# Kernel optimization log

Hardware: AMD Instinct MI355X
Metric: run time of the kernel (lower is better)

## Reference

```python
import jax, jax.numpy as jnp
import numpy as np

DEPTH, DIM, HEADS = 12, 768, 12
B, N = 2, 2048
HEAD_DIM = DIM // HEADS


def setup_inputs() -> dict:
    key = jax.random.key(0)
    ks = jax.random.split(key, 8)
    s = 0.02
    return {
        "x": jax.random.normal(ks[0], (B, N, DIM), jnp.float32),
        "sequence_ids": jnp.sort(jax.random.randint(ks[1], (B, N), 0, 8), axis=-1),
        "sequence_mask": jnp.zeros((B, N), dtype=bool),
        "ln1_w": jnp.ones((DEPTH, DIM), jnp.float32),
        "ln1_b": jnp.zeros((DEPTH, DIM), jnp.float32),
        "qkv_w": jax.random.normal(ks[2], (DEPTH, DIM, 3 * DIM), jnp.float32) * s,
        "qkv_b": jnp.zeros((DEPTH, 3 * DIM), jnp.float32),
        "proj_w": jax.random.normal(ks[3], (DEPTH, DIM, DIM), jnp.float32) * s,
        "proj_b": jnp.zeros((DEPTH, DIM), jnp.float32),
        "ls1_g": jnp.full((DEPTH, DIM), 1e-5, jnp.float32),
        "ln2_w": jnp.ones((DEPTH, DIM), jnp.float32),
        "ln2_b": jnp.zeros((DEPTH, DIM), jnp.float32),
        "fc1_w": jax.random.normal(ks[4], (DEPTH, DIM, 4 * DIM), jnp.float32) * s,
        "fc1_b": jnp.zeros((DEPTH, 4 * DIM), jnp.float32),
        "fc2_w": jax.random.normal(ks[5], (DEPTH, 4 * DIM, DIM), jnp.float32) * s,
        "fc2_b": jnp.zeros((DEPTH, DIM), jnp.float32),
        "ls2_g": jnp.full((DEPTH, DIM), 1e-5, jnp.float32),
        "r": 0,
    }


def _layernorm(x, w, b, eps=1e-5):
    m = x.mean(-1, keepdims=True)
    v = ((x - m) ** 2).mean(-1, keepdims=True)
    return (x - m) * jax.lax.rsqrt(v + eps) * w + b


def _attention(x, attn_mask, qkv_w, qkv_b, proj_w, proj_b):
    b, n, c = x.shape
    qkv = (x @ qkv_w + qkv_b).reshape(b, n, 3, HEADS, HEAD_DIM)
    qkv = jnp.transpose(qkv, (2, 0, 3, 1, 4))  # [3, B, H, N, hd]
    q, k, v = qkv[0], qkv[1], qkv[2]
    attn = jnp.einsum("bhqd,bhkd->bhqk", q, k) * (HEAD_DIM ** -0.5)
    neg_inf = jnp.finfo(attn.dtype).min
    attn = jnp.where(attn_mask[:, None, :, :], neg_inf, attn)  # broadcast over heads
    attn = jax.nn.softmax(attn, axis=-1)
    out = jnp.einsum("bhqk,bhkd->bhqd", attn, v)
    out = jnp.transpose(out, (0, 2, 1, 3)).reshape(b, n, c)
    return out @ proj_w + proj_b


def reference(x, sequence_ids, sequence_mask, ln1_w, ln1_b, qkv_w, qkv_b,
              proj_w, proj_b, ls1_g, ln2_w, ln2_b, fc1_w, fc1_b,
              fc2_w, fc2_b, ls2_g, r):
    # attn_mask: True where attention is NOT allowed
    attn_mask = sequence_ids[:, :, None] != sequence_ids[:, None, :]
    attn_mask = attn_mask | sequence_mask[:, :, None] | sequence_mask[:, None, :]
    for i in range(DEPTH):
        h = _layernorm(x, ln1_w[i], ln1_b[i])
        h = _attention(h, attn_mask, qkv_w[i], qkv_b[i], proj_w[i], proj_b[i])
        x = x + h * ls1_g[i]
        h = _layernorm(x, ln2_w[i], ln2_b[i])
        h = jax.nn.gelu(h @ fc1_w[i] + fc1_b[i], approximate=False) @ fc2_w[i] + fc2_b[i]
        x = x + h * ls2_g[i]
    return x
```

## Files before the change

kernel.cpp:

```cpp
#include <hip/hip_runtime.h>

#define NDEPTH 12
#define NDIM 768
#define NHEADS 12
#define NB 2
#define NSEQ 2048
#define MTOK (NB*NSEQ)

typedef short bf16x8 __attribute__((ext_vector_type(8)));
typedef float f32x4 __attribute__((ext_vector_type(4)));
typedef unsigned short u16;
typedef unsigned int u32;

#define L2E 1.44269504088896f

__device__ inline u16 f2bf(float f){
  union { float f; u32 u; } x; x.f = f;
  u32 r = x.u + 0x7fffu + ((x.u >> 16) & 1u);
  return (u16)(r >> 16);
}

__device__ inline f32x4 mfma16(bf16x8 a, bf16x8 b, f32x4 c){
  return __builtin_amdgcn_mfma_f32_16x16x32_bf16(a, b, c, 0, 0, 0);
}

#define GLOAD_LDS(gsrc, ldst) __builtin_amdgcn_global_load_lds( \
    (const __attribute__((address_space(1))) u32*)(gsrc), \
    (__attribute__((address_space(3))) u32*)(ldst), 16, 0, 0)

__device__ inline void ln_body(const float* __restrict__ x,
    const float* __restrict__ w, const float* __restrict__ b,
    u16* __restrict__ out, int blk){
  int wv = threadIdx.x >> 6, lane = threadIdx.x & 63;
  int row = blk * 4 + wv;
  const float* xr = x + (size_t)row * NDIM;
  float v[12];
  #pragma unroll
  for (int j = 0; j < 3; j++){
    float4 f = *(const float4*)&xr[4*lane + 256*j];
    v[j*4+0] = f.x; v[j*4+1] = f.y; v[j*4+2] = f.z; v[j*4+3] = f.w;
  }
  float s = 0.f;
  #pragma unroll
  for (int j = 0; j < 12; j++) s += v[j];
  #pragma unroll
  for (int m = 1; m < 64; m <<= 1) s += __shfl_xor(s, m);
  float mean = s * (1.0f/768.0f);
  float q = 0.f;
  #pragma unroll
  for (int j = 0; j < 12; j++){ float d = v[j]-mean; q += d*d; }
  #pragma unroll
  for (int m = 1; m < 64; m <<= 1) q += __shfl_xor(q, m);
  float rs = rsqrtf(q * (1.0f/768.0f) + 1e-5f);
  u16* orow = out + (size_t)row * NDIM;
  #pragma unroll
  for (int j = 0; j < 3; j++){
    int c0 = 4*lane + 256*j;
    u16 tmp[4];
    #pragma unroll
    for (int i = 0; i < 4; i++)
      tmp[i] = f2bf((v[j*4+i]-mean)*rs*w[c0+i] + b[c0+i]);
    *(uint2*)&orow[c0] = *(uint2*)tmp;
  }
}

__global__ __launch_bounds__(256) void ln_kernel(const float* __restrict__ x,
    const float* __restrict__ w, const float* __restrict__ b,
    u16* __restrict__ out){
  ln_body(x, w, b, out, blockIdx.x);
}

__device__ inline void wtrans_body(const float* __restrict__ in,
    u16* __restrict__ out, int K, int N, int n0, int k0, float* tile){
  int t = threadIdx.x;
  #pragma unroll
  for (int j = 0; j < 4; j++){
    int idx = t + j*256;
    int r = idx >> 4, c4 = (idx & 15) << 2;
    float4 f = *(const float4*)&in[(size_t)(k0+r)*N + n0 + c4];
    float* tp = &tile[r*65 + c4];
    tp[0] = f.x; tp[1] = f.y; tp[2] = f.z; tp[3] = f.w;
  }
  __syncthreads();
  #pragma unroll
  for (int j = 0; j < 2; j++){
    int idx = t + j*256;
    int c = idx >> 3, r8 = (idx & 7) << 3;
    u16 tmp[8];
    #pragma unroll
    for (int i = 0; i < 8; i++) tmp[i] = f2bf(tile[(r8+i)*65 + c]);
    *(uint4*)&out[(size_t)(n0+c)*K + k0 + r8] = *(uint4*)tmp;
  }
}

__global__ __launch_bounds__(256) void lnwt_kernel(
    const float* __restrict__ x, const float* __restrict__ lw,
    const float* __restrict__ lb, u16* __restrict__ lout,
    const float* __restrict__ qkvw, const float* __restrict__ projw,
    const float* __restrict__ fc1w, const float* __restrict__ fc2w,
    u16* __restrict__ wq, u16* __restrict__ wp,
    u16* __restrict__ w1, u16* __restrict__ w2){
  __shared__ float tile[64*65];
  int bid = blockIdx.x;
  if (bid < 1024){ ln_body(x, lw, lb, lout, bid); return; }
  bid -= 1024;
  const float* in; u16* out; int K, N, tl;
  if (bid < 432){        in = qkvw; out = wq; K = 768;  N = 2304; tl = bid; }
  else if (bid < 576){   in = projw; out = wp; K = 768; N = 768;  tl = bid - 432; }
  else if (bid < 1152){  in = fc1w; out = w1; K = 768;  N = 3072; tl = bid - 576; }
  else {                 in = fc2w; out = w2; K = 3072; N = 768;  tl = bid - 1152; }
  int ntn = N >> 6;
  int n0 = (tl % ntn) << 6, k0 = (tl / ntn) << 6;
  wtrans_body(in, out, K, N, n0, k0, tile);
}

__global__ __launch_bounds__(256) void wtrans_kernel(const float* __restrict__ in,
    u16* __restrict__ out, int K, int N){
  __shared__ float tile[64*65];
  wtrans_body(in, out, K, N, blockIdx.x*64, blockIdx.y*64, tile);
}

template<int BN, int EPI>
__global__ __launch_bounds__(512) void gemm_kernel(
    const u16* __restrict__ A, const u16* __restrict__ Wt,
    const float* __restrict__ bias, const float* __restrict__ g,
    u16* __restrict__ outb, float* __restrict__ xres,
    int M, int N, int K)
{
  constexpr int WGN = BN / 32;
  constexpr int WGM = 8 / WGN;
  constexpr int WTM = 128 / WGM;
  constexpr int MI = WTM / 16;
  constexpr int NI = 2;
  __shared__ u16 As[2][128*64];
  __shared__ u16 Bs[2][BN*64];
  int nwg = gridDim.x;
  int bid = (blockIdx.x & 7) * (nwg >> 3) + (blockIdx.x >> 3);
  int nt = N / BN;
  int bm = bid / nt, bn = bid % nt;
  int m0 = bm*128, n0 = bn*BN;
  int t = threadIdx.x, lane = t & 63, wv = t >> 6;
  int wm = (wv / WGN) * WTM, wn = (wv % WGN) * 32;
  f32x4 acc[MI][NI] = {};
  int fr = lane & 15, fg = lane >> 4;

  auto stage = [&](int bf, int k0){
    #pragma unroll
    for (int i = 0; i < 2; i++){
      int off = t*16 + i*8192;
      int row = off >> 7, cb = off & 127;
      const char* src = (const char*)A + ((size_t)(m0+row)*K + k0)*2 + (cb ^ ((row&7)<<4));
      GLOAD_LDS(src, (char*)As[bf] + off);
    }
    #pragma unroll
    for (int i = 0; i < BN/64; i++){
      int off = t*16 + i*8192;
      int row = off >> 7, cb = off & 127;
      const char* src = (const char*)Wt + ((size_t)(n0+row)*K + k0)*2 + (cb ^ ((row&7)<<4));
      GLOAD_LDS(src, (char*)Bs[bf] + off);
    }
  };

  stage(0, 0);
  int cur = 0;
  for (int k0 = 0; k0 < K; k0 += 64){
    __syncthreads();
    if (k0 + 64 < K) stage(cur ^ 1, k0 + 64);

    bf16x8 af[MI][2], bfv[NI][2];
    #pragma unroll
    for (int mi = 0; mi < MI; mi++)
      #pragma unroll
      for (int kh = 0; kh < 2; kh++){
        int row = wm + mi*16 + fr;
        int off = (row*128 + kh*64 + fg*16) ^ ((row&7)<<4);
        af[mi][kh] = *(const bf16x8*)((const char*)As[cur] + off);
      }
    #pragma unroll
    for (int ni = 0; ni < NI; ni++)
      #pragma unroll
      for (int kh = 0; kh < 2; kh++){
        int row = wn + ni*16 + fr;
        int off = (row*128 + kh*64 + fg*16) ^ ((row&7)<<4);
        bfv[ni][kh] = *(const bf16x8*)((const char*)Bs[cur] + off);
      }
    #pragma unroll
    for (int mi = 0; mi < MI; mi++)
      #pragma unroll
      for (int ni = 0; ni < NI; ni++){
        acc[mi][ni] = mfma16(af[mi][0], bfv[ni][0], acc[mi][ni]);
        acc[mi][ni] = mfma16(af[mi][1], bfv[ni][1], acc[mi][ni]);
      }
    cur ^= 1;
  }

  int fq = fg << 2;
  #pragma unroll
  for (int mi = 0; mi < MI; mi++){
    #pragma unroll
    for (int ni = 0; ni < NI; ni++){
      int col = n0 + wn + ni*16 + fr;
      float bv = bias[col];
      #pragma unroll
      for (int r = 0; r < 4; r++){
        int row = m0 + wm + mi*16 + fq + r;
        float v = acc[mi][ni][r] + bv;
        if (EPI == 0){
          outb[(size_t)row * N + col] = f2bf(v);
        } else if (EPI == 1){
          float ge = 0.5f * v * (1.0f + erff(v * 0.70710678118f));
          outb[(size_t)row * N + col] = f2bf(ge);
        } else {
          xres[(size_t)row * N + col] += v * g[col];
        }
      }
    }
  }
}

__global__ __launch_bounds__(256) void attn_kernel(
    const u16* __restrict__ qkv, const int* __restrict__ sid,
    const unsigned char* __restrict__ smask, u16* __restrict__ outb)
{
  __shared__ u16 Ks[64][72];
  __shared__ u16 Vs[64][72];
  __shared__ u16 Ps[4][16][72];
  int nwg = gridDim.x;
  int blk = (blockIdx.x & 7) * (nwg >> 3) + (blockIdx.x >> 3);
  int qt = blk & 31; int bh = blk >> 5;
  int b = bh / NHEADS, h = bh % NHEADS;
  int t = threadIdx.x, lane = t & 63, wv = t >> 6;
  int q0 = qt << 6;
  size_t rowbase = (size_t)b * NSEQ;
  int fr = lane & 15, fg8 = (lane >> 4) << 3, fq = (lane >> 4) << 2;

  int qrow = q0 + (wv << 4) + fr;
  const u16* qp = qkv + (rowbase + qrow) * 2304 + h*64 + fg8;
  bf16x8 qf0 = *(const bf16x8*)qp;
  bf16x8 qf1 = *(const bf16x8*)(qp + 32);

  int qlo = sid[rowbase + q0];
  int qhi = sid[rowbase + q0 + 63];

  int sq[4]; int mq[4];
  #pragma unroll
  for (int r = 0; r < 4; r++){
    int qr = q0 + (wv << 4) + fq + r;
    sq[r] = sid[rowbase + qr];
    mq[r] = smask[rowbase + qr];
  }
  float m[4], l[4]; f32x4 o[4] = {};
  #pragma unroll
  for (int r = 0; r < 4; r++){ m[r] = -3.0e38f; l[r] = 0.f; }

  int skk = t >> 2, sd = (t & 3) << 4;

  for (int kt = 0; kt < NSEQ/64; kt++){
    int klo = sid[rowbase + (kt << 6)];
    int khi = sid[rowbase + (kt << 6) + 63];
    if (khi < qlo || klo > qhi) continue;

    __syncthreads();
    int krow = (kt << 6) + skk;
    const u16* kp = qkv + (rowbase + krow) * 2304 + 768 + h*64 + sd;
    *(uint4*)&Ks[skk][sd]     = *(const uint4*)kp;
    *(uint4*)&Ks[skk][sd + 8] = *(const uint4*)(kp + 8);
    const u16* vp = kp + 768;
    uint4 v0 = *(const uint4*)vp, v1 = *(const uint4*)(vp + 8);
    {
      const u16* vv = (const u16*)&v0;
      #pragma unroll
      for (int i = 0; i < 8; i++) Vs[sd + i][skk] = vv[i];
      vv = (const u16*)&v1;
      #pragma unroll
      for (int i = 0; i < 8; i++) Vs[sd + 8 + i][skk] = vv[i];
    }
    int ks[4]; int mk[4];
    #pragma unroll
    for (int s2 = 0; s2 < 4; s2++){
      int kk = (kt << 6) + (s2 << 4) + fr;
      ks[s2] = sid[rowbase + kk];
      mk[s2] = smask[rowbase + kk];
    }
    __syncthreads();

    f32x4 S[4];
    #pragma unroll
    for (int s2 = 0; s2 < 4; s2++){
      bf16x8 kf0 = *(const bf16x8*)&Ks[(s2 << 4) + fr][fg8];
      bf16x8 kf1 = *(const bf16x8*)&Ks[(s2 << 4) + fr][fg8 + 32];
      f32x4 s = {};
      s = mfma16(qf0, kf0, s);
      s = mfma16(qf1, kf1, s);
      #pragma unroll
      for (int r = 0; r < 4; r++){
        float v = s[r] * 0.125f;
        bool msk = (mq[r] | mk[s2]) || (sq[r] != ks[s2]);
        S[s2][r] = msk ? -3.0e38f : v;
      }
    }
    float mn[4], sf[4], rs[4];
    #pragma unroll
    for (int r = 0; r < 4; r++){
      float mx = fmaxf(fmaxf(S[0][r], S[1][r]), fmaxf(S[2][r], S[3][r]));
      #pragma unroll
      for (int d = 1; d < 16; d <<= 1) mx = fmaxf(mx, __shfl_xor(mx, d));
      mn[r] = fmaxf(m[r], mx);
      sf[r] = exp2f((m[r] - mn[r]) * L2E);
      rs[r] = 0.f;
    }
    #pragma unroll
    for (int s2 = 0; s2 < 4; s2++){
      #pragma unroll
      for (int r = 0; r < 4; r++){
        float p = exp2f((S[s2][r] - mn[r]) * L2E);
        rs[r] += p;
        Ps[wv][fq + r][(s2 << 4) + fr] = f2bf(p);
      }
    }
    #pragma unroll
    for (int r = 0; r < 4; r++){
      #pragma unroll
      for (int d = 1; d < 16; d <<= 1) rs[r] += __shfl_xor(rs[r], d);
      l[r] = l[r] * sf[r] + rs[r];
      m[r] = mn[r];
    }
    #pragma unroll
    for (int dsub = 0; dsub < 4; dsub++)
      #pragma unroll
      for (int r = 0; r < 4; r++) o[dsub][r] *= sf[r];
    __syncthreads();
    #pragma unroll
    for (int kg = 0; kg < 2; kg++){
      bf16x8 pf = *(const bf16x8*)&Ps[wv][fr][(kg << 5) + fg8];
      #pragma unroll
      for (int dsub = 0; dsub < 4; dsub++){
        bf16x8 vf = *(const bf16x8*)&Vs[(dsub << 4) + fr][(kg << 5) + fg8];
        o[dsub] = mfma16(pf, vf, o[dsub]);
      }
    }
  }

  #pragma unroll
  for (int dsub = 0; dsub < 4; dsub++){
    #pragma unroll
    for (int r = 0; r < 4; r++){
      int row = q0 + (wv << 4) + fq + r;
      int col = h*64 + (dsub << 4) + fr;
      outb[(rowbase + row) * NDIM + col] = f2bf(o[dsub][r] / l[r]);
    }
  }
}

extern "C" void kernel_launch(void* const* d_in, const int* in_sizes, int n_in,
                              void* d_out, int out_size, void* d_ws, size_t ws_size,
                              hipStream_t stream) {
  const float* x_in = (const float*)d_in[0];
  const int* sid = (const int*)d_in[1];
  const unsigned char* smask = (const unsigned char*)d_in[2];
  const float* ln1w = (const float*)d_in[3];
  const float* ln1b = (const float*)d_in[4];
  const float* qkvw = (const float*)d_in[5];
  const float* qkvb = (const float*)d_in[6];
  const float* projw = (const float*)d_in[7];
  const float* projb = (const float*)d_in[8];
  const float* ls1 = (const float*)d_in[9];
  const float* ln2w = (const float*)d_in[10];
  const float* ln2b = (const float*)d_in[11];
  const float* fc1w = (const float*)d_in[12];
  const float* fc1b = (const float*)d_in[13];
  const float* fc2w = (const float*)d_in[14];
  const float* fc2b = (const float*)d_in[15];
  const float* ls2 = (const float*)d_in[16];

  float* x = (float*)d_out;
  char* ws = (char*)d_ws;
  u16* hbuf   = (u16*)ws;
  u16* qkvbuf = (u16*)(ws + (size_t)6291456);
  u16* abuf   = (u16*)(ws + (size_t)25165824);
  u16* mbuf   = (u16*)(ws + (size_t)31457280);
  const size_t WT0 = 56623104;

  bool fused_wt = ws_size >= WT0 + (size_t)14155776;
  u16* wall = (u16*)(ws + WT0);
  u16 *wq, *wp, *w1, *w2;
  if (fused_wt){
    wq = wall; wp = wq + (size_t)2304*768;
    w1 = wp + (size_t)768*768; w2 = w1 + (size_t)768*3072;
  } else {
    wq = wp = w1 = w2 = wall;
  }

  hipMemcpyAsync(x, x_in, (size_t)MTOK*NDIM*4, hipMemcpyDeviceToDevice, stream);

  for (int i = 0; i < NDEPTH; i++){
    const float* qw = qkvw + (size_t)i*NDIM*2304;
    const float* pw = projw + (size_t)i*NDIM*NDIM;
    const float* f1 = fc1w + (size_t)i*NDIM*3072;
    const float* f2 = fc2w + (size_t)i*3072*NDIM;

    if (fused_wt){
      lnwt_kernel<<<2752, 256, 0, stream>>>(x, ln1w + i*NDIM, ln1b + i*NDIM, hbuf,
                                            qw, pw, f1, f2, wq, wp, w1, w2);
    } else {
      ln_kernel<<<MTOK/4, 256, 0, stream>>>(x, ln1w + i*NDIM, ln1b + i*NDIM, hbuf);
      wtrans_kernel<<<dim3(2304/64, 768/64), 256, 0, stream>>>(qw, wq, NDIM, 2304);
    }
    gemm_kernel<128,0><<<(MTOK/128)*(2304/128), 512, 0, stream>>>(
        hbuf, wq, qkvb + (size_t)i*2304, nullptr, qkvbuf, nullptr, MTOK, 2304, NDIM);
    attn_kernel<<<NB*NHEADS*(NSEQ/64), 256, 0, stream>>>(qkvbuf, sid, smask, abuf);
    if (!fused_wt)
      wtrans_kernel<<<dim3(768/64, 768/64), 256, 0, stream>>>(pw, wp, NDIM, NDIM);
    gemm_kernel<64,2><<<(MTOK/128)*(NDIM/64), 512, 0, stream>>>(
        abuf, wp, projb + (size_t)i*NDIM, ls1 + (size_t)i*NDIM,
        nullptr, x, MTOK, NDIM, NDIM);
    ln_kernel<<<MTOK/4, 256, 0, stream>>>(x, ln2w + i*NDIM, ln2b + i*NDIM, hbuf);
    if (!fused_wt)
      wtrans_kernel<<<dim3(3072/64, 768/64), 256, 0, stream>>>(f1, w1, NDIM, 3072);
    gemm_kernel<128,1><<<(MTOK/128)*(3072/128), 512, 0, stream>>>(
        hbuf, w1, fc1b + (size_t)i*3072, nullptr, mbuf, nullptr, MTOK, 3072, NDIM);
    if (!fused_wt)
      wtrans_kernel<<<dim3(768/64, 3072/64), 256, 0, stream>>>(f2, w2, 3072, NDIM);
    gemm_kernel<64,2><<<(MTOK/128)*(NDIM/64), 512, 0, stream>>>(
        mbuf, w2, fc2b + (size_t)i*NDIM, ls2 + (size_t)i*NDIM,
        nullptr, x, MTOK, NDIM, 3072);
  }
}
```

Baseline: 2.080 ms.

## Switch dense GEMMs to FP8 operands with FP8 activations and weights

Converts layernorm outputs, attention outputs, GELU outputs and transposed weights to FP8 (e4m3 via v_cvt_pk_fp8_f32) and runs all four linear layers on the 16x16x32 FP8 MFMA. The LDS tiles and global loads are relaid for 1-byte elements with a smaller swizzle. This halves the bytes moved per GEMM and is meant to double MFMA throughput. It trades precision: the whole residual stream is fed through FP8 quantisation without scaling, which may exceed tolerance.

Measured after the change: 2.292 ms. +10.2%, slower.

```diff
diff --git a/kernel.cpp b/kernel.cpp
--- a/kernel.cpp
+++ b/kernel.cpp
@@ -11,6 +11,8 @@
 typedef float f32x4 __attribute__((ext_vector_type(4)));
 typedef unsigned short u16;
 typedef unsigned int u32;
+typedef unsigned char u8;
+typedef long long i64;
 
 #define L2E 1.44269504088896f
 
@@ -20,6 +22,12 @@
   return (u16)(r >> 16);
 }
 
+__device__ inline u32 cvt2fp8(float lo, float hi){
+  u32 r;
+  asm volatile("v_cvt_pk_fp8_f32 %0, %1, %2" : "=v"(r) : "v"(lo), "v"(hi));
+  return r & 0xffffu;
+}
+
 __device__ inline f32x4 mfma16(bf16x8 a, bf16x8 b, f32x4 c){
   return __builtin_amdgcn_mfma_f32_16x16x32_bf16(a, b, c, 0, 0, 0);
 }
@@ -30,7 +38,7 @@
 
 __device__ inline void ln_body(const float* __restrict__ x,
     const float* __restrict__ w, const float* __restrict__ b,
-    u16* __restrict__ out, int blk){
+    u8* __restrict__ out, int blk){
   int wv = threadIdx.x >> 6, lane = threadIdx.x & 63;
   int row = blk * 4 + wv;
   const float* xr = x + (size_t)row * NDIM;
@@ -52,26 +60,27 @@
   #pragma unroll
   for (int m = 1; m < 64; m <<= 1) q += __shfl_xor(q, m);
   float rs = rsqrtf(q * (1.0f/768.0f) + 1e-5f);
-  u16* orow = out + (size_t)row * NDIM;
+  u8* orow = out + (size_t)row * NDIM;
   #pragma unroll
   for (int j = 0; j < 3; j++){
     int c0 = 4*lane + 256*j;
-    u16 tmp[4];
-    #pragma unroll
-    for (int i = 0; i < 4; i++)
-      tmp[i] = f2bf((v[j*4+i]-mean)*rs*w[c0+i] + b[c0+i]);
-    *(uint2*)&orow[c0] = *(uint2*)tmp;
+    float y0 = (v[j*4+0]-mean)*rs*w[c0+0] + b[c0+0];
+    float y1 = (v[j*4+1]-mean)*rs*w[c0+1] + b[c0+1];
+    float y2 = (v[j*4+2]-mean)*rs*w[c0+2] + b[c0+2];
+    float y3 = (v[j*4+3]-mean)*rs*w[c0+3] + b[c0+3];
+    u32 lo = cvt2fp8(y0, y1), hi = cvt2fp8(y2, y3);
+    *(u32*)&orow[c0] = lo | (hi << 16);
   }
 }
 
 __global__ __launch_bounds__(256) void ln_kernel(const float* __restrict__ x,
     const float* __restrict__ w, const float* __restrict__ b,
-    u16* __restrict__ out){
+    u8* __restrict__ out){
   ln_body(x, w, b, out, blockIdx.x);
 }
 
 __device__ inline void wtrans_body(const float* __restrict__ in,
-    u16* __restrict__ out, int K, int N, int n0, int k0, float* tile){
+    u8* __restrict__ out, int K, int N, int n0, int k0, float* tile){
   int t = threadIdx.x;
   #pragma unroll
   for (int j = 0; j < 4; j++){
@@ -82,29 +91,30 @@
     tp[0] = f.x; tp[1] = f.y; tp[2] = f.z; tp[3] = f.w;
   }
   __syncthreads();
-  #pragma unroll
-  for (int j = 0; j < 2; j++){
-    int idx = t + j*256;
-    int c = idx >> 3, r8 = (idx & 7) << 3;
-    u16 tmp[8];
-    #pragma unroll
-    for (int i = 0; i < 8; i++) tmp[i] = f2bf(tile[(r8+i)*65 + c]);
-    *(uint4*)&out[(size_t)(n0+c)*K + k0 + r8] = *(uint4*)tmp;
-  }
+  int c = t >> 2, r16 = (t & 3) << 4;
+  u32 wds[4];
+  #pragma unroll
+  for (int p = 0; p < 4; p++){
+    u32 lo = cvt2fp8(tile[(r16+4*p+0)*65 + c], tile[(r16+4*p+1)*65 + c]);
+    u32 hi = cvt2fp8(tile[(r16+4*p+2)*65 + c], tile[(r16+4*p+3)*65 + c]);
+    wds[p] = lo | (hi << 16);
+  }
+  uint4 o; o.x = wds[0]; o.y = wds[1]; o.z = wds[2]; o.w = wds[3];
+  *(uint4*)&out[(size_t)(n0+c)*K + k0 + r16] = o;
 }
 
 __global__ __launch_bounds__(256) void lnwt_kernel(
     const float* __restrict__ x, const float* __restrict__ lw,
-    const float* __restrict__ lb, u16* __restrict__ lout,
+    const float* __restrict__ lb, u8* __restrict__ lout,
     const float* __restrict__ qkvw, const float* __restrict__ projw,
     const float* __restrict__ fc1w, const float* __restrict__ fc2w,
-    u16* __restrict__ wq, u16* __restrict__ wp,
-    u16* __restrict__ w1, u16* __restrict__ w2){
+    u8* __restrict__ wq, u8* __restrict__ wp,
+    u8* __restrict__ w1, u8* __restrict__ w2){
   __shared__ float tile[64*65];
   int bid = blockIdx.x;
   if (bid < 1024){ ln_body(x, lw, lb, lout, bid); return; }
   bid -= 1024;
-  const float* in; u16* out; int K, N, tl;
+  const float* in; u8* out; int K, N, tl;
   if (bid < 432){        in = qkvw; out = wq; K = 768;  N = 2304; tl = bid; }
   else if (bid < 576){   in = projw; out = wp; K = 768; N = 768;  tl = bid - 432; }
   else if (bid < 1152){  in = fc1w; out = w1; K = 768;  N = 3072; tl = bid - 576; }
@@ -115,16 +125,16 @@
 }
 
 __global__ __launch_bounds__(256) void wtrans_kernel(const float* __restrict__ in,
-    u16* __restrict__ out, int K, int N){
+    u8* __restrict__ out, int K, int N){
   __shared__ float tile[64*65];
   wtrans_body(in, out, K, N, blockIdx.x*64, blockIdx.y*64, tile);
 }
 
 template<int BN, int EPI>
-__global__ __launch_bounds__(512) void gemm_kernel(
-    const u16* __restrict__ A, const u16* __restrict__ Wt,
+__global__ __launch_bounds__(512) void gemm8_kernel(
+    const u8* __restrict__ A, const u8* __restrict__ Wt,
     const float* __restrict__ bias, const float* __restrict__ g,
-    u16* __restrict__ outb, float* __restrict__ xres,
+    u16* __restrict__ outb, u8* __restrict__ out8, float* __restrict__ xres,
     int M, int N, int K)
 {
   constexpr int WGN = BN / 32;
@@ -132,8 +142,8 @@
   constexpr int WTM = 128 / WGM;
   constexpr int MI = WTM / 16;
   constexpr int NI = 2;
-  __shared__ u16 As[2][128*64];
-  __shared__ u16 Bs[2][BN*64];
+  __shared__ u8 As[2][128*64];
+  __shared__ u8 Bs[2][BN*64];
   int nwg = gridDim.x;
   int bid = (blockIdx.x & 7) * (nwg >> 3) + (blockIdx.x >> 3);
   int nt = N / BN;
@@ -145,18 +155,16 @@
   int fr = lane & 15, fg = lane >> 4;
 
   auto stage = [&](int bf, int k0){
-    #pragma unroll
-    for (int i = 0; i < 2; i++){
-      int off = t*16 + i*8192;
-      int row = off >> 7, cb = off & 127;
-      const char* src = (const char*)A + ((size_t)(m0+row)*K + k0)*2 + (cb ^ ((row&7)<<4));
+    {
+      int off = t*16;
+      int row = off >> 6, cb = off & 63;
+      const char* src = (const char*)A + (size_t)(m0+row)*K + k0 + (cb ^ ((row&3)<<4));
       GLOAD_LDS(src, (char*)As[bf] + off);
     }
-    #pragma unroll
-    for (int i = 0; i < BN/64; i++){
-      int off = t*16 + i*8192;
-      int row = off >> 7, cb = off & 127;
-      const char* src = (const char*)Wt + ((size_t)(n0+row)*K + k0)*2 + (cb ^ ((row&7)<<4));
+    if (BN == 128 || t < 256){
+      int off = t*16;
+      int row = off >> 6, cb = off & 63;
+      const char* src = (const char*)Wt + (size_t)(n0+row)*K + k0 + (cb ^ ((row&3)<<4));
       GLOAD_LDS(src, (char*)Bs[bf] + off);
     }
   };
@@ -167,29 +175,29 @@
     __syncthreads();
     if (k0 + 64 < K) stage(cur ^ 1, k0 + 64);
 
-    bf16x8 af[MI][2], bfv[NI][2];
+    i64 af[MI][2], bfv[NI][2];
     #pragma unroll
     for (int mi = 0; mi < MI; mi++)
       #pragma unroll
       for (int kh = 0; kh < 2; kh++){
         int row = wm + mi*16 + fr;
-        int off = (row*128 + kh*64 + fg*16) ^ ((row&7)<<4);
-        af[mi][kh] = *(const bf16x8*)((const char*)As[cur] + off);
+        int off = row*64 + ((kh*32 + fg*8) ^ ((row&3)<<4));
+        af[mi][kh] = *(const i64*)&As[cur][off];
       }
     #pragma unroll
     for (int ni = 0; ni < NI; ni++)
       #pragma unroll
       for (int kh = 0; kh < 2; kh++){
         int row = wn + ni*16 + fr;
-        int off = (row*128 + kh*64 + fg*16) ^ ((row&7)<<4);
-        bfv[ni][kh] = *(const bf16x8*)((const char*)Bs[cur] + off);
+        int off = row*64 + ((kh*32 + fg*8) ^ ((row&3)<<4));
+        bfv[ni][kh] = *(const i64*)&Bs[cur][off];
       }
     #pragma unroll
     for (int mi = 0; mi < MI; mi++)
       #pragma unroll
       for (int ni = 0; ni < NI; ni++){
-        acc[mi][ni] = mfma16(af[mi][0], bfv[ni][0], acc[mi][ni]);
-        acc[mi][ni] = mfma16(af[mi][1], bfv[ni][1], acc[mi][ni]);
+        acc[mi][ni] = __builtin_amdgcn_mfma_f32_16x16x32_fp8_fp8(af[mi][0], bfv[ni][0], acc[mi][ni], 0, 0, 0);
+        acc[mi][ni] = __builtin_amdgcn_mfma_f32_16x16x32_fp8_fp8(af[mi][1], bfv[ni][1], acc[mi][ni], 0, 0, 0);
       }
     cur ^= 1;
   }
@@ -209,7 +217,7 @@
           outb[(size_t)row * N + col] = f2bf(v);
         } else if (EPI == 1){
           float ge = 0.5f * v * (1.0f + erff(v * 0.70710678118f));
-          outb[(size_t)row * N + col] = f2bf(ge);
+          out8[(size_t)row * N + col] = (u8)(cvt2fp8(ge, 0.f) & 0xff);
         } else {
           xres[(size_t)row * N + col] += v * g[col];
         }
@@ -220,7 +228,7 @@
 
 __global__ __launch_bounds__(256) void attn_kernel(
     const u16* __restrict__ qkv, const int* __restrict__ sid,
-    const unsigned char* __restrict__ smask, u16* __restrict__ outb)
+    const unsigned char* __restrict__ smask, u8* __restrict__ out8)
 {
   __shared__ u16 Ks[64][72];
   __shared__ u16 Vs[64][72];
@@ -347,7 +355,7 @@
     for (int r = 0; r < 4; r++){
       int row = q0 + (wv << 4) + fq + r;
       int col = h*64 + (dsub << 4) + fr;
-      outb[(rowbase + row) * NDIM + col] = f2bf(o[dsub][r] / l[r]);
+      out8[(rowbase + row) * NDIM + col] = (u8)(cvt2fp8(o[dsub][r] / l[r], 0.f) & 0xff);
     }
   }
 }
@@ -375,15 +383,15 @@
 
   float* x = (float*)d_out;
   char* ws = (char*)d_ws;
-  u16* hbuf   = (u16*)ws;
+  u8*  hbuf   = (u8*)ws;
   u16* qkvbuf = (u16*)(ws + (size_t)6291456);
-  u16* abuf   = (u16*)(ws + (size_t)25165824);
-  u16* mbuf   = (u16*)(ws + (size_t)31457280);
+  u8*  abuf   = (u8*)(ws + (size_t)25165824);
+  u8*  mbuf   = (u8*)(ws + (size_t)31457280);
   const size_t WT0 = 56623104;
 
-  bool fused_wt = ws_size >= WT0 + (size_t)14155776;
-  u16* wall = (u16*)(ws + WT0);
-  u16 *wq, *wp, *w1, *w2;
+  bool fused_wt = ws_size >= WT0 + (size_t)7077888;
+  u8* wall = (u8*)(ws + WT0);
+  u8 *wq, *wp, *w1, *w2;
   if (fused_wt){
     wq = wall; wp = wq + (size_t)2304*768;
     w1 = wp + (size_t)768*768; w2 = w1 + (size_t)768*3072;
@@ -406,23 +414,23 @@
       ln_kernel<<<MTOK/4, 256, 0, stream>>>(x, ln1w + i*NDIM, ln1b + i*NDIM, hbuf);
       wtrans_kernel<<<dim3(2304/64, 768/64), 256, 0, stream>>>(qw, wq, NDIM, 2304);
     }
-    gemm_kernel<128,0><<<(MTOK/128)*(2304/128), 512, 0, stream>>>(
-        hbuf, wq, qkvb + (size_t)i*2304, nullptr, qkvbuf, nullptr, MTOK, 2304, NDIM);
+    gemm8_kernel<128,0><<<(MTOK/128)*(2304/128), 512, 0, stream>>>(
+        hbuf, wq, qkvb + (size_t)i*2304, nullptr, qkvbuf, nullptr, nullptr, MTOK, 2304, NDIM);
     attn_kernel<<<NB*NHEADS*(NSEQ/64), 256, 0, stream>>>(qkvbuf, sid, smask, abuf);
     if (!fused_wt)
       wtrans_kernel<<<dim3(768/64, 768/64), 256, 0, stream>>>(pw, wp, NDIM, NDIM);
-    gemm_kernel<64,2><<<(MTOK/128)*(NDIM/64), 512, 0, stream>>>(
+    gemm8_kernel<64,2><<<(MTOK/128)*(NDIM/64), 512, 0, stream>>>(
         abuf, wp, projb + (size_t)i*NDIM, ls1 + (size_t)i*NDIM,
-        nullptr, x, MTOK, NDIM, NDIM);
+        nullptr, nullptr, x, MTOK, NDIM, NDIM);
     ln_kernel<<<MTOK/4, 256, 0, stream>>>(x, ln2w + i*NDIM, ln2b + i*NDIM, hbuf);
     if (!fused_wt)
       wtrans_kernel<<<dim3(3072/64, 768/64), 256, 0, stream>>>(f1, w1, NDIM, 3072);
-    gemm_kernel<128,1><<<(MTOK/128)*(3072/128), 512, 0, stream>>>(
-        hbuf, w1, fc1b + (size_t)i*3072, nullptr, mbuf, nullptr, MTOK, 3072, NDIM);
+    gemm8_kernel<128,1><<<(MTOK/128)*(3072/128), 512, 0, stream>>>(
+        hbuf, w1, fc1b + (size_t)i*3072, nullptr, nullptr, mbuf, nullptr, MTOK, 3072, NDIM);
     if (!fused_wt)
       wtrans_kernel<<<dim3(768/64, 3072/64), 256, 0, stream>>>(f2, w2, 3072, NDIM);
-    gemm_kernel<64,2><<<(MTOK/128)*(NDIM/64), 512, 0, stream>>>(
+    gemm8_kernel<64,2><<<(MTOK/128)*(NDIM/64), 512, 0, stream>>>(
         mbuf, w2, fc2b + (size_t)i*NDIM, ls2 + (size_t)i*NDIM,
-        nullptr, x, MTOK, NDIM, 3072);
-  }
-}
+        nullptr, nullptr, x, MTOK, NDIM, 3072);
+  }
+}
```

## Move proj/fc1/fc2 weight transposes into attention launch to overlap with attention

Applied to the files above, without the earlier changes.

Splits the weight-transpose work. The LN1 kernel now transposes only the QKV weights. The proj, fc1 and fc2 weight conversions move into a combined attention kernel whose extra blocks run alongside the attention blocks. This is meant to hide the memory-bound transpose work behind the compute-heavy attention and to shorten the LN+transpose launch that sits on the critical path before the QKV GEMM. Attention now uses one shared byte buffer carved into its K, V and P tiles, and the attention block swizzle is hardcoded for 1024 blocks.

New measurement: 5.980 ms. 2.88x slower.

```diff
diff --git a/kernel.cpp b/kernel.cpp
--- a/kernel.cpp
+++ b/kernel.cpp
@@ -93,25 +93,16 @@
   }
 }
 
-__global__ __launch_bounds__(256) void lnwt_kernel(
+__global__ __launch_bounds__(256) void lnqw_kernel(
     const float* __restrict__ x, const float* __restrict__ lw,
     const float* __restrict__ lb, u16* __restrict__ lout,
-    const float* __restrict__ qkvw, const float* __restrict__ projw,
-    const float* __restrict__ fc1w, const float* __restrict__ fc2w,
-    u16* __restrict__ wq, u16* __restrict__ wp,
-    u16* __restrict__ w1, u16* __restrict__ w2){
+    const float* __restrict__ qkvw, u16* __restrict__ wq){
   __shared__ float tile[64*65];
   int bid = blockIdx.x;
   if (bid < 1024){ ln_body(x, lw, lb, lout, bid); return; }
   bid -= 1024;
-  const float* in; u16* out; int K, N, tl;
-  if (bid < 432){        in = qkvw; out = wq; K = 768;  N = 2304; tl = bid; }
-  else if (bid < 576){   in = projw; out = wp; K = 768; N = 768;  tl = bid - 432; }
-  else if (bid < 1152){  in = fc1w; out = w1; K = 768;  N = 3072; tl = bid - 576; }
-  else {                 in = fc2w; out = w2; K = 3072; N = 768;  tl = bid - 1152; }
-  int ntn = N >> 6;
-  int n0 = (tl % ntn) << 6, k0 = (tl / ntn) << 6;
-  wtrans_body(in, out, K, N, n0, k0, tile);
+  int ntn = 2304 >> 6;
+  wtrans_body(qkvw, wq, 768, 2304, (bid % ntn) << 6, (bid / ntn) << 6, tile);
 }
 
 __global__ __launch_bounds__(256) void wtrans_kernel(const float* __restrict__ in,
@@ -218,15 +209,13 @@
   }
 }
 
-__global__ __launch_bounds__(256) void attn_kernel(
-    const u16* __restrict__ qkv, const int* __restrict__ sid,
-    const unsigned char* __restrict__ smask, u16* __restrict__ outb)
+__device__ void attn_body(const u16* __restrict__ qkv, const int* __restrict__ sid,
+    const unsigned char* __restrict__ smask, u16* __restrict__ outb,
+    int blk, char* smem)
 {
-  __shared__ u16 Ks[64][72];
-  __shared__ u16 Vs[64][72];
-  __shared__ u16 Ps[4][16][72];
-  int nwg = gridDim.x;
-  int blk = (blockIdx.x & 7) * (nwg >> 3) + (blockIdx.x >> 3);
+  u16 (*Ks)[72] = (u16(*)[72])smem;
+  u16 (*Vs)[72] = (u16(*)[72])(smem + 9216);
+  u16 (*Ps)[16][72] = (u16(*)[16][72])(smem + 18432);
   int qt = blk & 31; int bh = blk >> 5;
   int b = bh / NHEADS, h = bh % NHEADS;
   int t = threadIdx.x, lane = t & 63, wv = t >> 6;
@@ -350,6 +339,39 @@
       outb[(rowbase + row) * NDIM + col] = f2bf(o[dsub][r] / l[r]);
     }
   }
+}
+
+__global__ __launch_bounds__(256) void attnwt_kernel(
+    const u16* __restrict__ qkv, const int* __restrict__ sid,
+    const unsigned char* __restrict__ smask, u16* __restrict__ aout,
+    const float* __restrict__ projw, const float* __restrict__ fc1w,
+    const float* __restrict__ fc2w,
+    u16* __restrict__ wp, u16* __restrict__ w1, u16* __restrict__ w2)
+{
+  __shared__ char smem[27648];
+  int bid = blockIdx.x;
+  if (bid < 1024){
+    int blk = (bid & 7) * 128 + (bid >> 3);
+    attn_body(qkv, sid, smask, aout, blk, smem);
+    return;
+  }
+  bid -= 1024;
+  const float* in; u16* out; int K, N, tl;
+  if (bid < 144){       in = projw; out = wp; K = 768;  N = 768;  tl = bid; }
+  else if (bid < 720){  in = fc1w;  out = w1; K = 768;  N = 3072; tl = bid - 144; }
+  else {                in = fc2w;  out = w2; K = 3072; N = 768;  tl = bid - 720; }
+  int ntn = N >> 6;
+  wtrans_body(in, out, K, N, (tl % ntn) << 6, (tl / ntn) << 6, (float*)smem);
+}
+
+__global__ __launch_bounds__(256) void attn_kernel(
+    const u16* __restrict__ qkv, const int* __restrict__ sid,
+    const unsigned char* __restrict__ smask, u16* __restrict__ outb)
+{
+  __shared__ char smem[27648];
+  int nwg = gridDim.x;
+  int blk = (blockIdx.x & 7) * (nwg >> 3) + (blockIdx.x >> 3);
+  attn_body(qkv, sid, smask, outb, blk, smem);
 }
 
 extern "C" void kernel_launch(void* const* d_in, const int* in_sizes, int n_in,
@@ -400,17 +422,20 @@
     const float* f2 = fc2w + (size_t)i*3072*NDIM;
 
     if (fused_wt){
-      lnwt_kernel<<<2752, 256, 0, stream>>>(x, ln1w + i*NDIM, ln1b + i*NDIM, hbuf,
-                                            qw, pw, f1, f2, wq, wp, w1, w2);
+      lnqw_kernel<<<1456, 256, 0, stream>>>(x, ln1w + i*NDIM, ln1b + i*NDIM, hbuf, qw, wq);
     } else {
       ln_kernel<<<MTOK/4, 256, 0, stream>>>(x, ln1w + i*NDIM, ln1b + i*NDIM, hbuf);
       wtrans_kernel<<<dim3(2304/64, 768/64), 256, 0, stream>>>(qw, wq, NDIM, 2304);
     }
     gemm_kernel<128,0><<<(MTOK/128)*(2304/128), 512, 0, stream>>>(
         hbuf, wq, qkvb + (size_t)i*2304, nullptr, qkvbuf, nullptr, MTOK, 2304, NDIM);
-    attn_kernel<<<NB*NHEADS*(NSEQ/64), 256, 0, stream>>>(qkvbuf, sid, smask, abuf);
-    if (!fused_wt)
+    if (fused_wt){
+      attnwt_kernel<<<2320, 256, 0, stream>>>(qkvbuf, sid, smask, abuf,
+                                              pw, f1, f2, wp, w1, w2);
+    } else {
+      attn_kernel<<<NB*NHEADS*(NSEQ/64), 256, 0, stream>>>(qkvbuf, sid, smask, abuf);
       wtrans_kernel<<<dim3(768/64, 768/64), 256, 0, stream>>>(pw, wp, NDIM, NDIM);
+    }
     gemm_kernel<64,2><<<(MTOK/128)*(NDIM/64), 512, 0, stream>>>(
         abuf, wp, projb + (size_t)i*NDIM, ls1 + (size_t)i*NDIM,
         nullptr, x, MTOK, NDIM, NDIM);
```
